# Kernel tuning notes

Measured on AMD Instinct MI355X. Metric: run time of the kernel, lower is better.

## Reference

```python
import jax, jax.numpy as jnp
import numpy as np

N = 200000   # num nodes
E = 2500000  # num edges
H = 32       # hidden_dim
EPS = 1e-5   # BatchNorm eps


def _gcn_conv(x, W, b, src, dst, norm):
    # GCNConv: D^{-1/2}(A+I)D^{-1/2} X W + b  (self-loops folded in via norm^2 term)
    h = x @ W                                   # [N, H_out]
    coef = norm[src] * norm[dst]                # [E]
    msg = h[src] * coef[:, None]                # [E, H_out] -- dominant HBM traffic
    agg = jax.ops.segment_sum(msg, dst, num_segments=N)
    agg = agg + h * (norm * norm)[:, None]      # self-loop contribution
    return agg + b


def _bn(x, gamma, beta):
    # BatchNorm1d in training mode: batch statistics over the node dimension
    m = jnp.mean(x, axis=0)
    v = jnp.var(x, axis=0)
    return gamma * (x - m) * jax.lax.rsqrt(v + EPS) + beta


def setup_inputs() -> dict:
    key = jax.random.key(0)
    ks = jax.random.split(key, 12)
    x = jax.random.uniform(ks[0], (N, 1), dtype=jnp.float32) * 50.0  # degree-like feature
    edge_index = jax.random.randint(ks[1], (2, E), 0, N, dtype=jnp.int64)
    edge_attr = jax.random.normal(ks[2], (E,), dtype=jnp.float32)
    s = 0.1
    return {
        'x': x, 'edge_index': edge_index, 'edge_attr': edge_attr,
        'W1': jax.random.normal(ks[3], (1, H), dtype=jnp.float32) * s,
        'b1': jnp.zeros((H,), jnp.float32),
        'g1': jnp.ones((H,), jnp.float32), 'be1': jnp.zeros((H,), jnp.float32),
        'W2': jax.random.normal(ks[4], (H, H), dtype=jnp.float32) * s,
        'b2': jnp.zeros((H,), jnp.float32),
        'g2': jnp.ones((H,), jnp.float32), 'be2': jnp.zeros((H,), jnp.float32),
        'W3': jax.random.normal(ks[5], (H, H), dtype=jnp.float32) * s,
        'b3': jnp.zeros((H,), jnp.float32),
        'g3': jnp.ones((H,), jnp.float32), 'be3': jnp.zeros((H,), jnp.float32),
        'fcW': jax.random.normal(ks[6], (H, 1), dtype=jnp.float32) * s,
        'fcb': jnp.zeros((1,), jnp.float32),
    }


def reference(x, edge_index, edge_attr, W1, b1, g1, be1, W2, b2, g2, be2,
              W3, b3, g3, be3, fcW, fcb):
    src, dst = edge_index[0], edge_index[1]
    # symmetric normalization from degrees of A + I
    deg = jax.ops.segment_sum(jnp.ones((E,), x.dtype), dst, num_segments=N) + 1.0
    norm = jax.lax.rsqrt(deg)                   # deg^{-1/2}, [N]

    h = jax.nn.relu(_bn(_gcn_conv(x, W1, b1, src, dst, norm), g1, be1))
    h = jax.nn.relu(_bn(_gcn_conv(h, W2, b2, src, dst, norm), g2, be2))
    h = jax.nn.relu(_bn(_gcn_conv(h, W3, b3, src, dst, norm), g3, be3))
    # dropout is identity in eval / deterministic reference
    return h @ fcW + fcb                        # [N, 1]
```

## Files before the change

### kernel.cpp

```cpp
#include <hip/hip_runtime.h>
#include <hip/hip_bf16.h>
#include <hip/hip_fp16.h>

#define N_NODES 200000
#define N_EDGES 2500000
#define HID 32
#define BN_EPS 1e-5f

#define BKT_SHIFT 10
#define B_BKT ((N_NODES + 1023) / 1024)
#define PAD 16
#define CAPB 14336
#define EDGES_PER_BLK 8192
#define NB_SCAT ((N_EDGES + EDGES_PER_BLK - 1) / EDGES_PER_BLK)

#define SBANK 4096
#define SSTR 16
#define S1SUM 0
#define S1SQ  16
#define L2SUM 32
#define L2SQ  544
#define L3SUM 1056
#define L3SQ  1568

#define NB1  3125
#define NBL2 3125
#define ITL2 2
#define NBH  3125

typedef float nfloat4 __attribute__((ext_vector_type(4)));

__device__ __forceinline__ void atomAddF(float* p, float v) {
    unsafeAtomicAdd(p, v);
}

__device__ __forceinline__ void ntStore4(float* p, float a, float b, float c, float d) {
    nfloat4 v = {a, b, c, d};
    __builtin_nontemporal_store(v, (nfloat4*)p);
}

__global__ void k_init(int* __restrict__ bcur16, float* __restrict__ stats) {
    int i = blockIdx.x * blockDim.x + threadIdx.x;
    if (i < B_BKT * PAD) bcur16[i] = 0;
    if (i < 4 * SBANK) stats[i] = 0.0f;
}

__global__ void __launch_bounds__(1024)
k_scatter(const int* __restrict__ ei, int* __restrict__ bcur16,
          unsigned int* __restrict__ ebuf) {
    __shared__ int lh[B_BKT], lbase[B_BKT], lc[B_BKT];
    int t = threadIdx.x;
    if (t < B_BKT) { lh[t] = 0; lc[t] = 0; }
    __syncthreads();
    int base = blockIdx.x * EDGES_PER_BLK;
    int sv[8], dv[8];
#pragma unroll
    for (int k = 0; k < 8; k++) {
        int e = base + k * 1024 + t;
        if (e < N_EDGES) {
            sv[k] = ei[e];
            dv[k] = ei[N_EDGES + e];
            atomicAdd(&lh[dv[k] >> BKT_SHIFT], 1);
        } else dv[k] = -1;
    }
    __syncthreads();
    if (t < B_BKT) lbase[t] = lh[t] ? atomicAdd(&bcur16[t * PAD], lh[t]) : 0;
    __syncthreads();
#pragma unroll
    for (int k = 0; k < 8; k++) {
        if (dv[k] >= 0) {
            int b = dv[k] >> BKT_SHIFT;
            int loc = atomicAdd(&lc[b], 1);
            ebuf[(size_t)b * CAPB + lbase[b] + loc] =
                ((unsigned)(dv[k] & 1023) << 18) | (unsigned)sv[k];
        }
    }
}

__global__ void __launch_bounds__(1024)
k_bucket(const unsigned int* __restrict__ ebuf, const int* __restrict__ bcur16,
         const float* __restrict__ x, int* __restrict__ rowbeg,
         int* __restrict__ cntg, float* __restrict__ norm,
         float* __restrict__ xp, int* __restrict__ csrc) {
    __shared__ int hist[1024], rbase[1024];
    __shared__ int wsum[16];
    int b = blockIdx.x;
    int t = threadIdx.x;
    int lane = t & 63, wv = t >> 6;
    int count = bcur16[b * PAD];
    size_t ebase = (size_t)b * CAPB;
    int nbase = b << BKT_SHIFT;
    hist[t] = 0;
    __syncthreads();
    for (int i = t; i < count; i += 1024)
        atomicAdd(&hist[ebuf[ebase + i] >> 18], 1);
    __syncthreads();
    int v = hist[t];
    int val = v;
#pragma unroll
    for (int off = 1; off < 64; off <<= 1) {
        int nn = __shfl_up(val, off);
        if (lane >= off) val += nn;
    }
    if (lane == 63) wsum[wv] = val;
    __syncthreads();
    if (t < 16) {
        int wval = wsum[t];
        int wincl = wval;
#pragma unroll
        for (int off = 1; off < 16; off <<= 1) {
            int nn = __shfl_up(wincl, off, 16);
            if (t >= off) wincl += nn;
        }
        wsum[t] = wincl - wval;
    }
    __syncthreads();
    int excl = (val - v) + wsum[wv];
    int rb = b * CAPB + excl;
    rbase[t] = rb;
    int n = nbase + t;
    if (n < N_NODES) {
        rowbeg[n] = rb;
        cntg[n] = v;
        float nm = rsqrtf((float)v + 1.0f);
        norm[n] = nm;
        xp[n] = x[n] * nm;
    }
    __syncthreads();
    hist[t] = 0;
    __syncthreads();
    for (int i = t; i < count; i += 1024) {
        unsigned int w = ebuf[ebase + i];
        int ld = w >> 18;
        int loc = atomicAdd(&hist[ld], 1);
        csrc[rbase[ld] + loc] = (int)(w & 0x3FFFFu);
    }
}

__global__ void __launch_bounds__(256)
k_gather1(const int* __restrict__ rowbeg, const int* __restrict__ cntg,
          const int* __restrict__ csrc, const float* __restrict__ xp,
          const float* __restrict__ norm, float2* __restrict__ sn2,
          float* __restrict__ stats) {
    __shared__ float ls[256], lq[256];
    int tid = threadIdx.x;
    int nl = tid >> 2, q = tid & 3;
    int n = blockIdx.x * 64 + nl;
    int beg = rowbeg[n], dg = cntg[n];
    float A0 = 0.f, A1 = 0.f;
    int i = q;
    for (; i + 4 < dg; i += 8) {
        A0 += xp[__builtin_nontemporal_load(csrc + beg + i)];
        A1 += xp[__builtin_nontemporal_load(csrc + beg + i + 4)];
    }
    if (i < dg) A0 += xp[__builtin_nontemporal_load(csrc + beg + i)];
    float acc = A0 + A1;
    acc += __shfl_xor(acc, 1);
    acc += __shfl_xor(acc, 2);
    float val = 0.f;
    if (q == 0) {
        acc += xp[n];
        float nm = norm[n];
        val = nm * acc;
        sn2[n] = make_float2(val, nm);
    }
    ls[tid] = val; lq[tid] = val * val;
    __syncthreads();
    for (int off = 128; off; off >>= 1) {
        if (tid < (unsigned)off) { ls[tid] += ls[tid + off]; lq[tid] += lq[tid + off]; }
        __syncthreads();
    }
    if (tid == 0) {
        int bo = (blockIdx.x & 3) * SBANK;
        atomAddF(&stats[bo + S1SUM], ls[0]);
        atomAddF(&stats[bo + S1SQ],  lq[0]);
    }
}

#define PHI(aa, bb, pp) ((pp).y * fmaxf(fmaf((aa), (pp).x, (bb)), 0.f))

__global__ void __launch_bounds__(256)
k_layer2(const int* __restrict__ rowbeg, const int* __restrict__ cntg,
         const int* __restrict__ csrc, const float2* __restrict__ sn2,
         const float* __restrict__ stats, const float* __restrict__ W1,
         const float* __restrict__ g1, const float* __restrict__ be1,
         const float* __restrict__ W2, float* __restrict__ B,
         float* __restrict__ sumO, float* __restrict__ sqO) {
    __shared__ float w2s[1024];
    __shared__ float ajs[32], bjs[32];
    __shared__ float yx[32][36];
    __shared__ float red[4][8][8];
    int tid = threadIdx.x;
    for (int i = tid; i < 1024; i += 256) w2s[i] = W2[i];
    if (tid < 32) {
        float sm = stats[S1SUM] + stats[SBANK + S1SUM] +
                   stats[2*SBANK + S1SUM] + stats[3*SBANK + S1SUM];
        float sq = stats[S1SQ] + stats[SBANK + S1SQ] +
                   stats[2*SBANK + S1SQ] + stats[3*SBANK + S1SQ];
        float m   = sm * (1.0f / N_NODES);
        float var = sq * (1.0f / N_NODES) - m * m;
        float w = W1[tid];
        float a = g1[tid] * w * rsqrtf(var * w * w + BN_EPS);
        ajs[tid] = a;
        bjs[tid] = be1[tid] - m * a;
    }
    __syncthreads();
    int nl = tid >> 3, cg = (tid & 7) * 4;
    float a0 = ajs[cg], a1 = ajs[cg+1], a2 = ajs[cg+2], a3 = ajs[cg+3];
    float b0 = bjs[cg], b1 = bjs[cg+1], b2 = bjs[cg+2], b3 = bjs[cg+3];
    float s0=0,s1=0,s2=0,s3=0,q0=0,q1=0,q2=0,q3=0;
#pragma unroll
    for (int it = 0; it < ITL2; it++) {
        int n = (it * NBL2 + blockIdx.x) * 32 + nl;
        int beg = rowbeg[n], dg = cntg[n];
        float2 self = sn2[n];
        float nm = self.y;
        float h0 = PHI(a0,b0,self), h1 = PHI(a1,b1,self),
              h2 = PHI(a2,b2,self), h3 = PHI(a3,b3,self);
        int i = 0;
        for (; i + 3 < dg; i += 4) {
            int e0 = __builtin_nontemporal_load(csrc + beg + i);
            int e1 = __builtin_nontemporal_load(csrc + beg + i + 1);
            int e2 = __builtin_nontemporal_load(csrc + beg + i + 2);
            int e3 = __builtin_nontemporal_load(csrc + beg + i + 3);
            float2 p0 = sn2[e0], p1 = sn2[e1], p2 = sn2[e2], p3 = sn2[e3];
            h0 += PHI(a0,b0,p0) + PHI(a0,b0,p1) + PHI(a0,b0,p2) + PHI(a0,b0,p3);
            h1 += PHI(a1,b1,p0) + PHI(a1,b1,p1) + PHI(a1,b1,p2) + PHI(a1,b1,p3);
            h2 += PHI(a2,b2,p0) + PHI(a2,b2,p1) + PHI(a2,b2,p2) + PHI(a2,b2,p3);
            h3 += PHI(a3,b3,p0) + PHI(a3,b3,p1) + PHI(a3,b3,p2) + PHI(a3,b3,p3);
        }
        for (; i < dg; i++) {
            float2 p = sn2[__builtin_nontemporal_load(csrc + beg + i)];
            h0 += PHI(a0,b0,p); h1 += PHI(a1,b1,p);
            h2 += PHI(a2,b2,p); h3 += PHI(a3,b3,p);
        }
        __syncthreads();
        *(float4*)&yx[nl][cg] = make_float4(h0,h1,h2,h3);
        __syncthreads();
        float o0=0,o1=0,o2=0,o3=0;
#pragma unroll
        for (int k = 0; k < 32; k += 4) {
            float4 hh  = *(const float4*)&yx[nl][k];
            float4 wr0 = *(const float4*)&w2s[(k+0)*32 + cg];
            float4 wr1 = *(const float4*)&w2s[(k+1)*32 + cg];
            float4 wr2 = *(const float4*)&w2s[(k+2)*32 + cg];
            float4 wr3 = *(const float4*)&w2s[(k+3)*32 + cg];
            o0 = fmaf(hh.x,wr0.x, fmaf(hh.y,wr1.x, fmaf(hh.z,wr2.x, fmaf(hh.w,wr3.x, o0))));
            o1 = fmaf(hh.x,wr0.y, fmaf(hh.y,wr1.y, fmaf(hh.z,wr2.y, fmaf(hh.w,wr3.y, o1))));
            o2 = fmaf(hh.x,wr0.z, fmaf(hh.y,wr1.z, fmaf(hh.z,wr2.z, fmaf(hh.w,wr3.z, o2))));
            o3 = fmaf(hh.x,wr0.w, fmaf(hh.y,wr1.w, fmaf(hh.z,wr2.w, fmaf(hh.w,wr3.w, o3))));
        }
        o0 *= nm; o1 *= nm; o2 *= nm; o3 *= nm;
        ntStore4(B + (size_t)n * 32 + cg, o0, o1, o2, o3);
        s0 += o0; s1 += o1; s2 += o2; s3 += o3;
        q0 += o0*o0; q1 += o1*o1; q2 += o2*o2; q3 += o3*o3;
    }
#pragma unroll
    for (int mask = 32; mask >= 8; mask >>= 1) {
        s0 += __shfl_xor(s0, mask); s1 += __shfl_xor(s1, mask);
        s2 += __shfl_xor(s2, mask); s3 += __shfl_xor(s3, mask);
        q0 += __shfl_xor(q0, mask); q1 += __shfl_xor(q1, mask);
        q2 += __shfl_xor(q2, mask); q3 += __shfl_xor(q3, mask);
    }
    int wv = tid >> 6, ln = tid & 63;
    if (ln < 8) {
        float* r = red[wv][ln];
        r[0]=s0; r[1]=s1; r[2]=s2; r[3]=s3;
        r[4]=q0; r[5]=q1; r[6]=q2; r[7]=q3;
    }
    __syncthreads();
    if (tid < 8) {
        float tacc[8] = {0,0,0,0,0,0,0,0};
#pragma unroll
        for (int w = 0; w < 4; w++)
#pragma unroll
            for (int k = 0; k < 8; k++) tacc[k] += red[w][tid][k];
        int cb = tid * 4;
        int bo = (blockIdx.x & 3) * SBANK;
#pragma unroll
        for (int k = 0; k < 4; k++) {
            atomAddF(&sumO[bo + (cb + k) * SSTR], tacc[k]);
            atomAddF(&sqO [bo + (cb + k) * SSTR], tacc[4 + k]);
        }
    }
}

__global__ void __launch_bounds__(256)
k_fusedB(const float* __restrict__ norm, const float* __restrict__ sum,
         const float* __restrict__ sumsq, const float* __restrict__ g,
         const float* __restrict__ be, const float* __restrict__ W,
         const float* __restrict__ aggIn, __half* __restrict__ hOut) {
    __shared__ float wl[1024];
    __shared__ float scs[32], shs[32];
    __shared__ float yx[32][36];
    int tid = threadIdx.x;
    for (int i = tid; i < 1024; i += 256) wl[i] = W[i];
    if (tid < 32) {
        int o = tid * SSTR;
        float sm = sum[o] + sum[o+SBANK] + sum[o+2*SBANK] + sum[o+3*SBANK];
        float sq = sumsq[o] + sumsq[o+SBANK] + sumsq[o+2*SBANK] + sumsq[o+3*SBANK];
        float m   = sm * (1.0f / N_NODES);
        float var = sq * (1.0f / N_NODES) - m * m;
        float scj = g[tid] * rsqrtf(var + BN_EPS);
        scs[tid] = scj;
        shs[tid] = be[tid] - m * scj;
    }
    __syncthreads();
    int nl = tid >> 3, cg = (tid & 7) * 4;
    int n = blockIdx.x * 32 + nl;
    float4 bi = *(const float4*)(aggIn + (size_t)n * 32 + cg);
    float y0 = fmaxf(scs[cg  ]*bi.x + shs[cg  ], 0.f);
    float y1 = fmaxf(scs[cg+1]*bi.y + shs[cg+1], 0.f);
    float y2 = fmaxf(scs[cg+2]*bi.z + shs[cg+2], 0.f);
    float y3 = fmaxf(scs[cg+3]*bi.w + shs[cg+3], 0.f);
    *(float4*)&yx[nl][cg] = make_float4(y0,y1,y2,y3);
    __syncthreads();
    float o0=0,o1=0,o2=0,o3=0;
#pragma unroll
    for (int k = 0; k < 32; k += 4) {
        float4 hh  = *(const float4*)&yx[nl][k];
        float4 wr0 = *(const float4*)&wl[(k+0)*32 + cg];
        float4 wr1 = *(const float4*)&wl[(k+1)*32 + cg];
        float4 wr2 = *(const float4*)&wl[(k+2)*32 + cg];
        float4 wr3 = *(const float4*)&wl[(k+3)*32 + cg];
        o0 = fmaf(hh.x,wr0.x, fmaf(hh.y,wr1.x, fmaf(hh.z,wr2.x, fmaf(hh.w,wr3.x, o0))));
        o1 = fmaf(hh.x,wr0.y, fmaf(hh.y,wr1.y, fmaf(hh.z,wr2.y, fmaf(hh.w,wr3.y, o1))));
        o2 = fmaf(hh.x,wr0.z, fmaf(hh.y,wr1.z, fmaf(hh.z,wr2.z, fmaf(hh.w,wr3.z, o2))));
        o3 = fmaf(hh.x,wr0.w, fmaf(hh.y,wr1.w, fmaf(hh.z,wr2.w, fmaf(hh.w,wr3.w, o3))));
    }
    float nm = norm[n];
    __half2 ha = __floats2half2_rn(o0 * nm, o1 * nm);
    __half2 hb = __floats2half2_rn(o2 * nm, o3 * nm);
    float2 pk;
    ((__half2*)&pk)[0] = ha;
    ((__half2*)&pk)[1] = hb;
    *(float2*)(hOut + (size_t)n * 32 + cg) = pk;
}

__device__ __forceinline__ void acc8(float* a, float4 raw) {
    const __half2* h = (const __half2*)&raw;
    float2 f0 = __half22float2(h[0]);
    float2 f1 = __half22float2(h[1]);
    float2 f2 = __half22float2(h[2]);
    float2 f3 = __half22float2(h[3]);
    a[0] += f0.x; a[1] += f0.y; a[2] += f1.x; a[3] += f1.y;
    a[4] += f2.x; a[5] += f2.y; a[6] += f3.x; a[7] += f3.y;
}

__global__ void __launch_bounds__(256)
k_gatherH(const int* __restrict__ rowbeg, const int* __restrict__ cntg,
          const int* __restrict__ csrc, const __half* __restrict__ A,
          const float* __restrict__ norm, float* __restrict__ B,
          float* __restrict__ sum, float* __restrict__ sumsq) {
    int tid = threadIdx.x;
    int nl = tid >> 2;
    int c8 = (tid & 3) * 8;
    int n = blockIdx.x * 64 + nl;
    int beg = rowbeg[n], dg = cntg[n];
    const __half* Ac = A + c8;
    float acc[8] = {0,0,0,0,0,0,0,0};
    acc8(acc, *(const float4*)(Ac + (size_t)n * 32));
    int i = 0;
    for (; i + 3 < dg; i += 4) {
        int e0 = __builtin_nontemporal_load(csrc + beg + i);
        int e1 = __builtin_nontemporal_load(csrc + beg + i + 1);
        int e2 = __builtin_nontemporal_load(csrc + beg + i + 2);
        int e3 = __builtin_nontemporal_load(csrc + beg + i + 3);
        float4 r0 = *(const float4*)(Ac + (size_t)e0 * 32);
        float4 r1 = *(const float4*)(Ac + (size_t)e1 * 32);
        float4 r2 = *(const float4*)(Ac + (size_t)e2 * 32);
        float4 r3 = *(const float4*)(Ac + (size_t)e3 * 32);
        acc8(acc, r0); acc8(acc, r1); acc8(acc, r2); acc8(acc, r3);
    }
    if (i + 1 < dg) {
        int e0 = __builtin_nontemporal_load(csrc + beg + i);
        int e1 = __builtin_nontemporal_load(csrc + beg + i + 1);
        float4 r0 = *(const float4*)(Ac + (size_t)e0 * 32);
        float4 r1 = *(const float4*)(Ac + (size_t)e1 * 32);
        acc8(acc, r0); acc8(acc, r1);
        i += 2;
    }
    if (i < dg) {
        int e0 = __builtin_nontemporal_load(csrc + beg + i);
        acc8(acc, *(const float4*)(Ac + (size_t)e0 * 32));
    }
    float nm = norm[n];
    float o[8];
#pragma unroll
    for (int k = 0; k < 8; k++) o[k] = acc[k] * nm;
    ntStore4(B + (size_t)n * 32 + c8,     o[0], o[1], o[2], o[3]);
    ntStore4(B + (size_t)n * 32 + c8 + 4, o[4], o[5], o[6], o[7]);
    float st[16];
#pragma unroll
    for (int k = 0; k < 8; k++) { st[k] = o[k]; st[8 + k] = o[k] * o[k]; }
#pragma unroll
    for (int mask = 32; mask >= 4; mask >>= 1)
#pragma unroll
        for (int k = 0; k < 16; k++) st[k] += __shfl_xor(st[k], mask);
    __shared__ float red[4][4][16];
    int wv = tid >> 6, ln = tid & 63;
    if (ln < 4) {
#pragma unroll
        for (int k = 0; k < 16; k++) red[wv][ln][k] = st[k];
    }
    __syncthreads();
    if (tid < 4) {
        float tacc[16];
#pragma unroll
        for (int k = 0; k < 16; k++) tacc[k] = 0.f;
#pragma unroll
        for (int w = 0; w < 4; w++)
#pragma unroll
            for (int k = 0; k < 16; k++) tacc[k] += red[w][tid][k];
        int cb = tid * 8;
        int bo = (blockIdx.x & 3) * SBANK;
#pragma unroll
        for (int k = 0; k < 8; k++) {
            atomAddF(&sum[bo + (cb + k) * SSTR], tacc[k]);
            atomAddF(&sumsq[bo + (cb + k) * SSTR], tacc[8 + k]);
        }
    }
}

__global__ void __launch_bounds__(256)
k_final(const float* __restrict__ aggIn, const float* __restrict__ sum,
        const float* __restrict__ sumsq, const float* __restrict__ g,
        const float* __restrict__ be, const float* __restrict__ fcW,
        const float* __restrict__ fcb, float* __restrict__ out) {
    __shared__ float scs[32], shs[32], fws[32];
    int tid = threadIdx.x;
    if (tid < 32) {
        int o = tid * SSTR;
        float sm = sum[o] + sum[o+SBANK] + sum[o+2*SBANK] + sum[o+3*SBANK];
        float sq = sumsq[o] + sumsq[o+SBANK] + sumsq[o+2*SBANK] + sumsq[o+3*SBANK];
        float m   = sm * (1.0f / N_NODES);
        float var = sq * (1.0f / N_NODES) - m * m;
        float scj = g[tid] * rsqrtf(var + BN_EPS);
        scs[tid] = scj;
        shs[tid] = be[tid] - m * scj;
        fws[tid] = fcW[tid];
    }
    __syncthreads();
    int nl = tid >> 3, cg = (tid & 7) * 4;
    int n = blockIdx.x * 32 + nl;
    float4 bi = *(const float4*)(aggIn + (size_t)n * 32 + cg);
    float v = fmaxf(scs[cg  ]*bi.x + shs[cg  ], 0.f) * fws[cg  ]
            + fmaxf(scs[cg+1]*bi.y + shs[cg+1], 0.f) * fws[cg+1]
            + fmaxf(scs[cg+2]*bi.z + shs[cg+2], 0.f) * fws[cg+2]
            + fmaxf(scs[cg+3]*bi.w + shs[cg+3], 0.f) * fws[cg+3];
    v += __shfl_xor(v, 1);
    v += __shfl_xor(v, 2);
    v += __shfl_xor(v, 4);
    if ((tid & 7) == 0) out[n] = v + fcb[0];
}

extern "C" void kernel_launch(void* const* d_in, const int* in_sizes, int n_in,
                              void* d_out, int out_size, void* d_ws, size_t ws_size,
                              hipStream_t stream) {
    const float* x   = (const float*)d_in[0];
    const int*   ei  = (const int*)d_in[1];
    const float* W1  = (const float*)d_in[3];
    const float* g1  = (const float*)d_in[5];
    const float* be1 = (const float*)d_in[6];
    const float* W2  = (const float*)d_in[7];
    const float* g2  = (const float*)d_in[9];
    const float* be2 = (const float*)d_in[10];
    const float* W3  = (const float*)d_in[11];
    const float* g3  = (const float*)d_in[13];
    const float* be3 = (const float*)d_in[14];
    const float* fcW = (const float*)d_in[15];
    const float* fcb = (const float*)d_in[16];
    float* out = (float*)d_out;

    char* base = (char*)d_ws;
    __half*       A16  = (__half*)base;
    unsigned int* ebuf = (unsigned int*)base;
    float*  B      = (float*)(base + (size_t)N_NODES * 32 * 4);
    int*    csrc   = (int*)(base + (size_t)N_NODES * 32 * 8);
    int*    rowbeg = csrc + (size_t)B_BKT * CAPB;
    int*    cntg   = rowbeg + N_NODES;
    float*  norm   = (float*)(cntg + N_NODES);
    float*  xp     = norm + N_NODES;
    float2* sn2    = (float2*)(xp + N_NODES);
    float*  stats  = (float*)(sn2 + N_NODES);
    int*    bcur16 = (int*)(stats + 4 * SBANK);

    k_init   <<<64, 256, 0, stream>>>(bcur16, stats);
    k_scatter<<<NB_SCAT, 1024, 0, stream>>>(ei, bcur16, ebuf);
    k_bucket <<<B_BKT, 1024, 0, stream>>>(ebuf, bcur16, x, rowbeg, cntg, norm, xp, csrc);
    k_gather1<<<NB1, 256, 0, stream>>>(rowbeg, cntg, csrc, xp, norm, sn2, stats);
    k_layer2 <<<NBL2, 256, 0, stream>>>(rowbeg, cntg, csrc, sn2, stats,
                                        W1, g1, be1, W2, B,
                                        stats + L2SUM, stats + L2SQ);
    k_fusedB <<<6250, 256, 0, stream>>>(norm, stats + L2SUM, stats + L2SQ,
                                        g2, be2, W3, B, A16);
    k_gatherH<<<NBH, 256, 0, stream>>>(rowbeg, cntg, csrc, A16, norm, B,
                                       stats + L3SUM, stats + L3SQ);
    k_final  <<<6250, 256, 0, stream>>>(B, stats + L3SUM, stats + L3SQ,
                                        g3, be3, fcW, fcb, out);
}
```

Measured before the change: 319.0 us.

## Replace bucketed CSR build with degree atomics, scan, and atomic placement

Replaces the two-pass bucket scatter/sort CSR construction with a global degree-count kernel using atomics, a per-bucket scan, and an atomic-cursor placement kernel that writes source ids directly into CSR slots. Row starts are recovered as rowbeg minus degree after placement. The gather kernels are also reworked: layer 1 and layer 2 now use 8 lanes per node with shuffle reductions and edge-parallel loops, and the half-precision gather uses masked 8-wide unrolled loads. This removes the intermediate edge buffer pass, but adds contended global atomics and gives a nondeterministic edge order within each row.

```diff
diff --git a/kernel.cpp b/kernel.cpp
--- a/kernel.cpp
+++ b/kernel.cpp
@@ -9,10 +9,7 @@
 
 #define BKT_SHIFT 10
 #define B_BKT ((N_NODES + 1023) / 1024)
-#define PAD 16
 #define CAPB 14336
-#define EDGES_PER_BLK 8192
-#define NB_SCAT ((N_EDGES + EDGES_PER_BLK - 1) / EDGES_PER_BLK)
 
 #define SBANK 4096
 #define SSTR 16
@@ -23,12 +20,11 @@
 #define L3SUM 1056
 #define L3SQ  1568
 
-#define NB1  3125
-#define NBL2 3125
-#define ITL2 2
-#define NBH  3125
+#define NBN32 6250
+#define NBH   3125
 
 typedef float nfloat4 __attribute__((ext_vector_type(4)));
+typedef int   nint4   __attribute__((ext_vector_type(4)));
 
 __device__ __forceinline__ void atomAddF(float* p, float v) {
     unsafeAtomicAdd(p, v);
@@ -39,63 +35,34 @@
     __builtin_nontemporal_store(v, (nfloat4*)p);
 }
 
-__global__ void k_init(int* __restrict__ bcur16, float* __restrict__ stats) {
+__global__ void k_init(int* __restrict__ cntg, float* __restrict__ stats) {
     int i = blockIdx.x * blockDim.x + threadIdx.x;
-    if (i < B_BKT * PAD) bcur16[i] = 0;
+    if (i < N_NODES) cntg[i] = 0;
     if (i < 4 * SBANK) stats[i] = 0.0f;
 }
 
+__global__ void __launch_bounds__(256)
+k_deg(const int* __restrict__ ei, int* __restrict__ cntg) {
+    const nint4* d4 = (const nint4*)(ei + N_EDGES);
+    int nc = N_EDGES / 4;
+    for (int c = blockIdx.x * 256 + threadIdx.x; c < nc; c += gridDim.x * 256) {
+        nint4 d = __builtin_nontemporal_load(d4 + c);
+        atomicAdd(&cntg[d[0]], 1);
+        atomicAdd(&cntg[d[1]], 1);
+        atomicAdd(&cntg[d[2]], 1);
+        atomicAdd(&cntg[d[3]], 1);
+    }
+}
+
 __global__ void __launch_bounds__(1024)
-k_scatter(const int* __restrict__ ei, int* __restrict__ bcur16,
-          unsigned int* __restrict__ ebuf) {
-    __shared__ int lh[B_BKT], lbase[B_BKT], lc[B_BKT];
-    int t = threadIdx.x;
-    if (t < B_BKT) { lh[t] = 0; lc[t] = 0; }
-    __syncthreads();
-    int base = blockIdx.x * EDGES_PER_BLK;
-    int sv[8], dv[8];
-#pragma unroll
-    for (int k = 0; k < 8; k++) {
-        int e = base + k * 1024 + t;
-        if (e < N_EDGES) {
-            sv[k] = ei[e];
-            dv[k] = ei[N_EDGES + e];
-            atomicAdd(&lh[dv[k] >> BKT_SHIFT], 1);
-        } else dv[k] = -1;
-    }
-    __syncthreads();
-    if (t < B_BKT) lbase[t] = lh[t] ? atomicAdd(&bcur16[t * PAD], lh[t]) : 0;
-    __syncthreads();
-#pragma unroll
-    for (int k = 0; k < 8; k++) {
-        if (dv[k] >= 0) {
-            int b = dv[k] >> BKT_SHIFT;
-            int loc = atomicAdd(&lc[b], 1);
-            ebuf[(size_t)b * CAPB + lbase[b] + loc] =
-                ((unsigned)(dv[k] & 1023) << 18) | (unsigned)sv[k];
-        }
-    }
-}
-
-__global__ void __launch_bounds__(1024)
-k_bucket(const unsigned int* __restrict__ ebuf, const int* __restrict__ bcur16,
-         const float* __restrict__ x, int* __restrict__ rowbeg,
-         int* __restrict__ cntg, float* __restrict__ norm,
-         float* __restrict__ xp, int* __restrict__ csrc) {
-    __shared__ int hist[1024], rbase[1024];
+k_scanN(const int* __restrict__ cntg, const float* __restrict__ x,
+        int* __restrict__ rowbeg, float* __restrict__ norm,
+        float* __restrict__ xp) {
     __shared__ int wsum[16];
-    int b = blockIdx.x;
-    int t = threadIdx.x;
+    int b = blockIdx.x, t = threadIdx.x;
     int lane = t & 63, wv = t >> 6;
-    int count = bcur16[b * PAD];
-    size_t ebase = (size_t)b * CAPB;
-    int nbase = b << BKT_SHIFT;
-    hist[t] = 0;
-    __syncthreads();
-    for (int i = t; i < count; i += 1024)
-        atomicAdd(&hist[ebuf[ebase + i] >> 18], 1);
-    __syncthreads();
-    int v = hist[t];
+    int n = (b << BKT_SHIFT) + t;
+    int v = (n < N_NODES) ? cntg[n] : 0;
     int val = v;
 #pragma unroll
     for (int off = 1; off < 64; off <<= 1) {
@@ -116,24 +83,27 @@
     }
     __syncthreads();
     int excl = (val - v) + wsum[wv];
-    int rb = b * CAPB + excl;
-    rbase[t] = rb;
-    int n = nbase + t;
     if (n < N_NODES) {
-        rowbeg[n] = rb;
-        cntg[n] = v;
+        rowbeg[n] = b * CAPB + excl;
         float nm = rsqrtf((float)v + 1.0f);
         norm[n] = nm;
         xp[n] = x[n] * nm;
     }
-    __syncthreads();
-    hist[t] = 0;
-    __syncthreads();
-    for (int i = t; i < count; i += 1024) {
-        unsigned int w = ebuf[ebase + i];
-        int ld = w >> 18;
-        int loc = atomicAdd(&hist[ld], 1);
-        csrc[rbase[ld] + loc] = (int)(w & 0x3FFFFu);
+}
+
+__global__ void __launch_bounds__(256)
+k_place(const int* __restrict__ ei, int* __restrict__ rowbeg,
+        int* __restrict__ csrc) {
+    const nint4* s4 = (const nint4*)ei;
+    const nint4* d4 = (const nint4*)(ei + N_EDGES);
+    int nc = N_EDGES / 4;
+    for (int c = blockIdx.x * 256 + threadIdx.x; c < nc; c += gridDim.x * 256) {
+        nint4 s = __builtin_nontemporal_load(s4 + c);
+        nint4 d = __builtin_nontemporal_load(d4 + c);
+        csrc[atomicAdd(&rowbeg[d[0]], 1)] = s[0];
+        csrc[atomicAdd(&rowbeg[d[1]], 1)] = s[1];
+        csrc[atomicAdd(&rowbeg[d[2]], 1)] = s[2];
+        csrc[atomicAdd(&rowbeg[d[3]], 1)] = s[3];
     }
 }
 
@@ -144,19 +114,21 @@
           float* __restrict__ stats) {
     __shared__ float ls[256], lq[256];
     int tid = threadIdx.x;
-    int nl = tid >> 2, q = tid & 3;
-    int n = blockIdx.x * 64 + nl;
-    int beg = rowbeg[n], dg = cntg[n];
+    int nl = tid >> 3, q = tid & 7;
+    int n = blockIdx.x * 32 + nl;
+    int dg = cntg[n];
+    int beg = rowbeg[n] - dg;
     float A0 = 0.f, A1 = 0.f;
     int i = q;
-    for (; i + 4 < dg; i += 8) {
+    for (; i + 8 < dg; i += 16) {
         A0 += xp[__builtin_nontemporal_load(csrc + beg + i)];
-        A1 += xp[__builtin_nontemporal_load(csrc + beg + i + 4)];
+        A1 += xp[__builtin_nontemporal_load(csrc + beg + i + 8)];
     }
     if (i < dg) A0 += xp[__builtin_nontemporal_load(csrc + beg + i)];
     float acc = A0 + A1;
     acc += __shfl_xor(acc, 1);
     acc += __shfl_xor(acc, 2);
+    acc += __shfl_xor(acc, 4);
     float val = 0.f;
     if (q == 0) {
         acc += xp[n];
@@ -176,8 +148,6 @@
         atomAddF(&stats[bo + S1SQ],  lq[0]);
     }
 }
-
-#define PHI(aa, bb, pp) ((pp).y * fmaxf(fmaf((aa), (pp).x, (bb)), 0.f))
 
 __global__ void __launch_bounds__(256)
 k_layer2(const int* __restrict__ rowbeg, const int* __restrict__ cntg,
@@ -187,7 +157,7 @@
          const float* __restrict__ W2, float* __restrict__ B,
          float* __restrict__ sumO, float* __restrict__ sqO) {
     __shared__ float w2s[1024];
-    __shared__ float ajs[32], bjs[32];
+    __shared__ __align__(16) float ajs[32], bjs[32];
     __shared__ float yx[32][36];
     __shared__ float red[4][8][8];
     int tid = threadIdx.x;
@@ -205,56 +175,64 @@
         bjs[tid] = be1[tid] - m * a;
     }
     __syncthreads();
-    int nl = tid >> 3, cg = (tid & 7) * 4;
-    float a0 = ajs[cg], a1 = ajs[cg+1], a2 = ajs[cg+2], a3 = ajs[cg+3];
-    float b0 = bjs[cg], b1 = bjs[cg+1], b2 = bjs[cg+2], b3 = bjs[cg+3];
-    float s0=0,s1=0,s2=0,s3=0,q0=0,q1=0,q2=0,q3=0;
-#pragma unroll
-    for (int it = 0; it < ITL2; it++) {
-        int n = (it * NBL2 + blockIdx.x) * 32 + nl;
-        int beg = rowbeg[n], dg = cntg[n];
-        float2 self = sn2[n];
-        float nm = self.y;
-        float h0 = PHI(a0,b0,self), h1 = PHI(a1,b1,self),
-              h2 = PHI(a2,b2,self), h3 = PHI(a3,b3,self);
-        int i = 0;
-        for (; i + 3 < dg; i += 4) {
-            int e0 = __builtin_nontemporal_load(csrc + beg + i);
-            int e1 = __builtin_nontemporal_load(csrc + beg + i + 1);
-            int e2 = __builtin_nontemporal_load(csrc + beg + i + 2);
-            int e3 = __builtin_nontemporal_load(csrc + beg + i + 3);
-            float2 p0 = sn2[e0], p1 = sn2[e1], p2 = sn2[e2], p3 = sn2[e3];
-            h0 += PHI(a0,b0,p0) + PHI(a0,b0,p1) + PHI(a0,b0,p2) + PHI(a0,b0,p3);
-            h1 += PHI(a1,b1,p0) + PHI(a1,b1,p1) + PHI(a1,b1,p2) + PHI(a1,b1,p3);
-            h2 += PHI(a2,b2,p0) + PHI(a2,b2,p1) + PHI(a2,b2,p2) + PHI(a2,b2,p3);
-            h3 += PHI(a3,b3,p0) + PHI(a3,b3,p1) + PHI(a3,b3,p2) + PHI(a3,b3,p3);
-        }
-        for (; i < dg; i++) {
-            float2 p = sn2[__builtin_nontemporal_load(csrc + beg + i)];
-            h0 += PHI(a0,b0,p); h1 += PHI(a1,b1,p);
-            h2 += PHI(a2,b2,p); h3 += PHI(a3,b3,p);
-        }
-        __syncthreads();
-        *(float4*)&yx[nl][cg] = make_float4(h0,h1,h2,h3);
-        __syncthreads();
-        float o0=0,o1=0,o2=0,o3=0;
-#pragma unroll
-        for (int k = 0; k < 32; k += 4) {
-            float4 hh  = *(const float4*)&yx[nl][k];
-            float4 wr0 = *(const float4*)&w2s[(k+0)*32 + cg];
-            float4 wr1 = *(const float4*)&w2s[(k+1)*32 + cg];
-            float4 wr2 = *(const float4*)&w2s[(k+2)*32 + cg];
-            float4 wr3 = *(const float4*)&w2s[(k+3)*32 + cg];
-            o0 = fmaf(hh.x,wr0.x, fmaf(hh.y,wr1.x, fmaf(hh.z,wr2.x, fmaf(hh.w,wr3.x, o0))));
-            o1 = fmaf(hh.x,wr0.y, fmaf(hh.y,wr1.y, fmaf(hh.z,wr2.y, fmaf(hh.w,wr3.y, o1))));
-            o2 = fmaf(hh.x,wr0.z, fmaf(hh.y,wr1.z, fmaf(hh.z,wr2.z, fmaf(hh.w,wr3.z, o2))));
-            o3 = fmaf(hh.x,wr0.w, fmaf(hh.y,wr1.w, fmaf(hh.z,wr2.w, fmaf(hh.w,wr3.w, o3))));
-        }
-        o0 *= nm; o1 *= nm; o2 *= nm; o3 *= nm;
-        ntStore4(B + (size_t)n * 32 + cg, o0, o1, o2, o3);
-        s0 += o0; s1 += o1; s2 += o2; s3 += o3;
-        q0 += o0*o0; q1 += o1*o1; q2 += o2*o2; q3 += o3*o3;
-    }
+    int nl = tid >> 3, l = tid & 7, cg = l * 4;
+    int n = blockIdx.x * 32 + nl;
+    int dg = cntg[n];
+    int beg = rowbeg[n] - dg;
+    float2 self = sn2[n];
+    float nm = self.y;
+    float h[32];
+#pragma unroll
+    for (int k = 0; k < 32; k++) h[k] = 0.f;
+    if (l == 0) {
+#pragma unroll
+        for (int k4 = 0; k4 < 32; k4 += 4) {
+            float4 a4 = *(const float4*)&ajs[k4];
+            float4 b4 = *(const float4*)&bjs[k4];
+            h[k4+0] = nm * fmaxf(fmaf(a4.x, self.x, b4.x), 0.f);
+            h[k4+1] = nm * fmaxf(fmaf(a4.y, self.x, b4.y), 0.f);
+            h[k4+2] = nm * fmaxf(fmaf(a4.z, self.x, b4.z), 0.f);
+            h[k4+3] = nm * fmaxf(fmaf(a4.w, self.x, b4.w), 0.f);
+        }
+    }
+    for (int i = l; i < dg; i += 8) {
+        float2 p = sn2[__builtin_nontemporal_load(csrc + beg + i)];
+        float w = p.y;
+#pragma unroll
+        for (int k4 = 0; k4 < 32; k4 += 4) {
+            float4 a4 = *(const float4*)&ajs[k4];
+            float4 b4 = *(const float4*)&bjs[k4];
+            h[k4+0] = fmaf(fmaxf(fmaf(a4.x, p.x, b4.x), 0.f), w, h[k4+0]);
+            h[k4+1] = fmaf(fmaxf(fmaf(a4.y, p.x, b4.y), 0.f), w, h[k4+1]);
+            h[k4+2] = fmaf(fmaxf(fmaf(a4.z, p.x, b4.z), 0.f), w, h[k4+2]);
+            h[k4+3] = fmaf(fmaxf(fmaf(a4.w, p.x, b4.w), 0.f), w, h[k4+3]);
+        }
+    }
+#pragma unroll
+    for (int k = 0; k < 32; k++) {
+        h[k] += __shfl_xor(h[k], 1);
+        h[k] += __shfl_xor(h[k], 2);
+        h[k] += __shfl_xor(h[k], 4);
+    }
+    *(float4*)&yx[nl][cg] = make_float4(h[cg], h[cg+1], h[cg+2], h[cg+3]);
+    __syncthreads();
+    float o0=0,o1=0,o2=0,o3=0;
+#pragma unroll
+    for (int k = 0; k < 32; k += 4) {
+        float4 hh  = *(const float4*)&yx[nl][k];
+        float4 wr0 = *(const float4*)&w2s[(k+0)*32 + cg];
+        float4 wr1 = *(const float4*)&w2s[(k+1)*32 + cg];
+        float4 wr2 = *(const float4*)&w2s[(k+2)*32 + cg];
+        float4 wr3 = *(const float4*)&w2s[(k+3)*32 + cg];
+        o0 = fmaf(hh.x,wr0.x, fmaf(hh.y,wr1.x, fmaf(hh.z,wr2.x, fmaf(hh.w,wr3.x, o0))));
+        o1 = fmaf(hh.x,wr0.y, fmaf(hh.y,wr1.y, fmaf(hh.z,wr2.y, fmaf(hh.w,wr3.y, o1))));
+        o2 = fmaf(hh.x,wr0.z, fmaf(hh.y,wr1.z, fmaf(hh.z,wr2.z, fmaf(hh.w,wr3.z, o2))));
+        o3 = fmaf(hh.x,wr0.w, fmaf(hh.y,wr1.w, fmaf(hh.z,wr2.w, fmaf(hh.w,wr3.w, o3))));
+    }
+    o0 *= nm; o1 *= nm; o2 *= nm; o3 *= nm;
+    ntStore4(B + (size_t)n * 32 + cg, o0, o1, o2, o3);
+    float s0 = o0, s1 = o1, s2 = o2, s3 = o3;
+    float q0 = o0*o0, q1 = o1*o1, q2 = o2*o2, q3 = o3*o3;
 #pragma unroll
     for (int mask = 32; mask >= 8; mask >>= 1) {
         s0 += __shfl_xor(s0, mask); s1 += __shfl_xor(s1, mask);
@@ -347,6 +325,18 @@
     a[4] += f2.x; a[5] += f2.y; a[6] += f3.x; a[7] += f3.y;
 }
 
+__device__ __forceinline__ void acc8m(float* a, float4 raw, float m) {
+    const __half2* h = (const __half2*)&raw;
+    float2 f0 = __half22float2(h[0]);
+    float2 f1 = __half22float2(h[1]);
+    float2 f2 = __half22float2(h[2]);
+    float2 f3 = __half22float2(h[3]);
+    a[0] = fmaf(m, f0.x, a[0]); a[1] = fmaf(m, f0.y, a[1]);
+    a[2] = fmaf(m, f1.x, a[2]); a[3] = fmaf(m, f1.y, a[3]);
+    a[4] = fmaf(m, f2.x, a[4]); a[5] = fmaf(m, f2.y, a[5]);
+    a[6] = fmaf(m, f3.x, a[6]); a[7] = fmaf(m, f3.y, a[7]);
+}
+
 __global__ void __launch_bounds__(256)
 k_gatherH(const int* __restrict__ rowbeg, const int* __restrict__ cntg,
           const int* __restrict__ csrc, const __half* __restrict__ A,
@@ -356,33 +346,35 @@
     int nl = tid >> 2;
     int c8 = (tid & 3) * 8;
     int n = blockIdx.x * 64 + nl;
-    int beg = rowbeg[n], dg = cntg[n];
+    int dg = cntg[n];
+    int beg = rowbeg[n] - dg;
     const __half* Ac = A + c8;
     float acc[8] = {0,0,0,0,0,0,0,0};
     acc8(acc, *(const float4*)(Ac + (size_t)n * 32));
-    int i = 0;
-    for (; i + 3 < dg; i += 4) {
-        int e0 = __builtin_nontemporal_load(csrc + beg + i);
-        int e1 = __builtin_nontemporal_load(csrc + beg + i + 1);
-        int e2 = __builtin_nontemporal_load(csrc + beg + i + 2);
-        int e3 = __builtin_nontemporal_load(csrc + beg + i + 3);
-        float4 r0 = *(const float4*)(Ac + (size_t)e0 * 32);
-        float4 r1 = *(const float4*)(Ac + (size_t)e1 * 32);
-        float4 r2 = *(const float4*)(Ac + (size_t)e2 * 32);
-        float4 r3 = *(const float4*)(Ac + (size_t)e3 * 32);
-        acc8(acc, r0); acc8(acc, r1); acc8(acc, r2); acc8(acc, r3);
-    }
-    if (i + 1 < dg) {
-        int e0 = __builtin_nontemporal_load(csrc + beg + i);
-        int e1 = __builtin_nontemporal_load(csrc + beg + i + 1);
-        float4 r0 = *(const float4*)(Ac + (size_t)e0 * 32);
-        float4 r1 = *(const float4*)(Ac + (size_t)e1 * 32);
-        acc8(acc, r0); acc8(acc, r1);
-        i += 2;
-    }
-    if (i < dg) {
-        int e0 = __builtin_nontemporal_load(csrc + beg + i);
-        acc8(acc, *(const float4*)(Ac + (size_t)e0 * 32));
+    int iters = (dg + 7) >> 3;
+    for (int t = 0; t < iters; t++) {
+        int i0 = t * 8;
+        int e[8]; float m[8];
+#pragma unroll
+        for (int j = 0; j < 8; j++) {
+            int idx = i0 + j;
+            bool ok = idx < dg;
+            int ic = ok ? idx : dg - 1;
+            e[j] = __builtin_nontemporal_load(csrc + beg + ic);
+            m[j] = ok ? 1.f : 0.f;
+        }
+        float4 r0 = *(const float4*)(Ac + (size_t)e[0] * 32);
+        float4 r1 = *(const float4*)(Ac + (size_t)e[1] * 32);
+        float4 r2 = *(const float4*)(Ac + (size_t)e[2] * 32);
+        float4 r3 = *(const float4*)(Ac + (size_t)e[3] * 32);
+        float4 r4 = *(const float4*)(Ac + (size_t)e[4] * 32);
+        float4 r5 = *(const float4*)(Ac + (size_t)e[5] * 32);
+        float4 r6 = *(const float4*)(Ac + (size_t)e[6] * 32);
+        float4 r7 = *(const float4*)(Ac + (size_t)e[7] * 32);
+        acc8m(acc, r0, m[0]); acc8m(acc, r1, m[1]);
+        acc8m(acc, r2, m[2]); acc8m(acc, r3, m[3]);
+        acc8m(acc, r4, m[4]); acc8m(acc, r5, m[5]);
+        acc8m(acc, r6, m[6]); acc8m(acc, r7, m[7]);
     }
     float nm = norm[n];
     float o[8];
@@ -473,8 +465,7 @@
     float* out = (float*)d_out;
 
     char* base = (char*)d_ws;
-    __half*       A16  = (__half*)base;
-    unsigned int* ebuf = (unsigned int*)base;
+    __half* A16    = (__half*)base;
     float*  B      = (float*)(base + (size_t)N_NODES * 32 * 4);
     int*    csrc   = (int*)(base + (size_t)N_NODES * 32 * 8);
     int*    rowbeg = csrc + (size_t)B_BKT * CAPB;
@@ -483,19 +474,19 @@
     float*  xp     = norm + N_NODES;
     float2* sn2    = (float2*)(xp + N_NODES);
     float*  stats  = (float*)(sn2 + N_NODES);
-    int*    bcur16 = (int*)(stats + 4 * SBANK);
-
-    k_init   <<<64, 256, 0, stream>>>(bcur16, stats);
-    k_scatter<<<NB_SCAT, 1024, 0, stream>>>(ei, bcur16, ebuf);
-    k_bucket <<<B_BKT, 1024, 0, stream>>>(ebuf, bcur16, x, rowbeg, cntg, norm, xp, csrc);
-    k_gather1<<<NB1, 256, 0, stream>>>(rowbeg, cntg, csrc, xp, norm, sn2, stats);
-    k_layer2 <<<NBL2, 256, 0, stream>>>(rowbeg, cntg, csrc, sn2, stats,
-                                        W1, g1, be1, W2, B,
-                                        stats + L2SUM, stats + L2SQ);
-    k_fusedB <<<6250, 256, 0, stream>>>(norm, stats + L2SUM, stats + L2SQ,
-                                        g2, be2, W3, B, A16);
+
+    k_init   <<<784, 256, 0, stream>>>(cntg, stats);
+    k_deg    <<<2048, 256, 0, stream>>>(ei, cntg);
+    k_scanN  <<<B_BKT, 1024, 0, stream>>>(cntg, x, rowbeg, norm, xp);
+    k_place  <<<2048, 256, 0, stream>>>(ei, rowbeg, csrc);
+    k_gather1<<<NBN32, 256, 0, stream>>>(rowbeg, cntg, csrc, xp, norm, sn2, stats);
+    k_layer2 <<<NBN32, 256, 0, stream>>>(rowbeg, cntg, csrc, sn2, stats,
+                                         W1, g1, be1, W2, B,
+                                         stats + L2SUM, stats + L2SQ);
+    k_fusedB <<<NBN32, 256, 0, stream>>>(norm, stats + L2SUM, stats + L2SQ,
+                                         g2, be2, W3, B, A16);
     k_gatherH<<<NBH, 256, 0, stream>>>(rowbeg, cntg, csrc, A16, norm, B,
                                        stats + L3SUM, stats + L3SQ);
-    k_final  <<<6250, 256, 0, stream>>>(B, stats + L3SUM, stats + L3SQ,
-                                        g3, be3, fcW, fcb, out);
-}
+    k_final  <<<NBN32, 256, 0, stream>>>(B, stats + L3SUM, stats + L3SQ,
+                                         g3, be3, fcW, fcb, out);
+}
```

Measured after the change: 596.1 us. 1.87x slower.
